# Optimization experiments

Hardware: AMD Instinct MI355X
Metric: run time of the kernel (lower is better)

## Reference

```python
import jax, jax.numpy as jnp
import numpy as np

N, IN_F, OUT_F = 65536, 512, 512


def setup_inputs() -> dict:
    key = jax.random.key(0)
    k1, k2, k3 = jax.random.split(key, 3)
    # Activations arrive as dequant-pending uint8-valued floats in [0, 256).
    x = jax.random.randint(k1, (N, IN_F), 0, 256).astype(jnp.float32)
    weight = jax.random.randint(k2, (OUT_F, IN_F), 0, 256).astype(jnp.int32)
    bias = jax.random.randint(k3, (OUT_F,), -512, 512).astype(jnp.int32)
    return {
        "x": x,
        "weight": weight,
        "bias": bias,
        "M": jnp.asarray(0.0123, dtype=jnp.float32),
        "x_zero": jnp.asarray(128.0, dtype=jnp.float32),
        "w_zero": jnp.asarray(128.0, dtype=jnp.float32),
        "y_zero": jnp.asarray(128.0, dtype=jnp.float32),
    }


def reference(x, weight, bias, M, x_zero, w_zero, y_zero):
    # y = round(linear(x - x_zero, w - w_zero, b) * M + y_zero)
    xs = x - x_zero                                   # [N, IN_F]
    w = weight.astype(jnp.float32) - w_zero           # [OUT_F, IN_F]
    y = jnp.einsum("ni,oi->no", xs, w) + bias.astype(jnp.float32)
    return jnp.round(y * M + y_zero)
```

## Files before the change

kernel.cpp:

```cpp
#include <hip/hip_runtime.h>


#define K_DIM 512
#define OUTF  512
#define NT    8
#define LDAB  80
#define TILE_B (128 * LDAB)
#define BUF_B  (2 * TILE_B)

typedef __attribute__((ext_vector_type(4))) int   i32x4;
typedef __attribute__((ext_vector_type(4))) float f32x4;

__global__ void wprep(const int* __restrict__ W, unsigned int* __restrict__ Wb,
                      const float* __restrict__ wzp) {
    const int wz = __float2int_rn(wzp[0]);
    int idx = (blockIdx.x * blockDim.x + threadIdx.x) * 4;
    i32x4 w = *reinterpret_cast<const i32x4*>(W + idx);
    unsigned int p = ((unsigned int)(w[0] - wz) & 0xffu)
                   | (((unsigned int)(w[1] - wz) & 0xffu) << 8)
                   | (((unsigned int)(w[2] - wz) & 0xffu) << 16)
                   | (((unsigned int)(w[3] - wz) & 0xffu) << 24);
    Wb[idx >> 2] = p;
}

__global__ __launch_bounds__(512, 4)
void qgemm(const float* __restrict__ X,
           const unsigned char* __restrict__ Wb,
           const int* __restrict__ bias,
           const float* __restrict__ Mp,
           const float* __restrict__ xzp,
           const float* __restrict__ yzp,
           float* __restrict__ Y) {
    __shared__ unsigned char lds[2 * BUF_B];

    const int tid  = threadIdx.x;
    const int lane = tid & 63;
    const int wid  = tid >> 6;
    const int wr   = wid >> 2;
    const int wc   = wid & 3;
    const int fr   = lane & 15;
    const int fq   = lane >> 4;

    const int b = blockIdx.x;
    const int lid = (b & 7) * 256 + (b >> 3);
    const int row0 = (lid >> 2) * 128;
    const int n0   = (lid & 3) * 128;

    const int xz = __float2int_rn(xzp[0]);

    const int srow = tid >> 2;
    const int scol = (tid & 3) * 16;
    const float* xbase = X + (size_t)(row0 + srow) * K_DIM + scol;
    const unsigned char* wbase = Wb + (size_t)(n0 + srow) * K_DIM + scol;
    const int aoff = srow * LDAB + scol;
    const int boff = TILE_B + srow * LDAB + scol;

    f32x4 ra[2][4];
    i32x4 rb[2];

    auto stage = [&](int t, int s) {
        const float* xp = xbase + t * 64;
        #pragma unroll
        for (int q = 0; q < 4; ++q)
            ra[s][q] = *reinterpret_cast<const f32x4*>(xp + q * 4);
        rb[s] = *reinterpret_cast<const i32x4*>(wbase + t * 64);
    };
    auto convwrite = [&](int buf, int s) {
        const int ab = buf * BUF_B;
        i32x4 pa;
        #pragma unroll
        for (int q = 0; q < 4; ++q) {
            unsigned int u0 = (unsigned int)((int)ra[s][q][0] - xz) & 0xffu;
            unsigned int u1 = (unsigned int)((int)ra[s][q][1] - xz) & 0xffu;
            unsigned int u2 = (unsigned int)((int)ra[s][q][2] - xz) & 0xffu;
            unsigned int u3 = (unsigned int)((int)ra[s][q][3] - xz) & 0xffu;
            pa[q] = (int)(u0 | (u1 << 8) | (u2 << 16) | (u3 << 24));
        }
        *reinterpret_cast<i32x4*>(&lds[ab + aoff]) = pa;
        *reinterpret_cast<i32x4*>(&lds[ab + boff]) = rb[s];
    };

    const int c0 = n0 + wc * 32;
    const int bv0 = bias[c0 + fr];
    const int bv1 = bias[c0 + 16 + fr];
    i32x4 acc[4][2];
    #pragma unroll
    for (int m = 0; m < 4; ++m) {
        acc[m][0] = i32x4{bv0, bv0, bv0, bv0};
        acc[m][1] = i32x4{bv1, bv1, bv1, bv1};
    }

    const int aro = (wr * 64 + fr) * LDAB + fq * 16;
    const int bro = TILE_B + (wc * 32 + fr) * LDAB + fq * 16;

    auto compute = [&](int buf) {
        const int ab = buf * BUF_B;
        i32x4 af[4], bf[2];
        #pragma unroll
        for (int m = 0; m < 4; ++m)
            af[m] = *reinterpret_cast<const i32x4*>(&lds[ab + aro + m * 16 * LDAB]);
        #pragma unroll
        for (int n = 0; n < 2; ++n)
            bf[n] = *reinterpret_cast<const i32x4*>(&lds[ab + bro + n * 16 * LDAB]);
        #pragma unroll
        for (int m = 0; m < 4; ++m)
            #pragma unroll
            for (int n = 0; n < 2; ++n)
                acc[m][n] = __builtin_amdgcn_mfma_i32_16x16x64_i8(
                    af[m], bf[n], acc[m][n], 0, 0, 0);
    };

    stage(0, 0);
    stage(1, 1);
    convwrite(0, 0);
    __syncthreads();

    #pragma unroll
    for (int t = 0; t < NT; ++t) {
        if (t + 2 < NT) stage(t + 2, t & 1);
        compute(t & 1);
        if (t + 1 < NT) convwrite((t + 1) & 1, (t + 1) & 1);
        __syncthreads();
    }

    const float Mv = Mp[0], yz = yzp[0];
    #pragma unroll
    for (int n = 0; n < 2; ++n) {
        const int col = c0 + n * 16 + fr;
        #pragma unroll
        for (int m = 0; m < 4; ++m) {
            const int row = row0 + wr * 64 + m * 16 + fq * 4;
            float* yp = Y + (size_t)row * OUTF + col;
            #pragma unroll
            for (int j = 0; j < 4; ++j)
                __builtin_nontemporal_store(
                    rintf((float)acc[m][n][j] * Mv + yz), yp + (size_t)j * OUTF);
        }
    }
}

extern "C" void kernel_launch(void* const* d_in, const int* in_sizes, int n_in,
                              void* d_out, int out_size, void* d_ws, size_t ws_size,
                              hipStream_t stream) {
    const float* x    = (const float*)d_in[0];
    const int*   w    = (const int*)d_in[1];
    const int*   bias = (const int*)d_in[2];
    const float* M    = (const float*)d_in[3];
    const float* xz   = (const float*)d_in[4];
    const float* wz   = (const float*)d_in[5];
    const float* yz   = (const float*)d_in[6];
    float* y = (float*)d_out;

    unsigned int* Wb = (unsigned int*)d_ws;

    wprep<<<256, 256, 0, stream>>>(w, Wb, wz);
    qgemm<<<2048, 512, 0, stream>>>(x, (const unsigned char*)Wb, bias, M, xz, yz, y);
}
```

Before: 68.67 us.

## Retile GEMM to 64-row blocks with full-width N and weights read from global

Each block now handles 64 rows across all 512 output columns, with each wave owning 64 columns. The weight fragments are loaded straight from global/L2 instead of being staged through LDS. The A tile is written to LDS in an MFMA-fragment-ordered layout so every lane reads a contiguous 16 bytes, and the barrier is replaced with an explicit lgkmcnt wait plus s_barrier. The aim is to read X exactly once, shrink LDS traffic and remove padding, but each wave now fetches weights from cache on every k-step and register pressure rises with 16 accumulators. Nontemporal stores are also dropped in favour of plain stores.

```diff
diff --git a/kernel.cpp b/kernel.cpp
--- a/kernel.cpp
+++ b/kernel.cpp
@@ -4,12 +4,10 @@
 #define K_DIM 512
 #define OUTF  512
 #define NT    8
-#define LDAB  80
-#define TILE_B (128 * LDAB)
-#define BUF_B  (2 * TILE_B)
 
 typedef __attribute__((ext_vector_type(4))) int   i32x4;
 typedef __attribute__((ext_vector_type(4))) float f32x4;
+typedef __attribute__((ext_vector_type(2))) unsigned int u32x2;
 
 __global__ void wprep(const int* __restrict__ W, unsigned int* __restrict__ Wb,
                       const float* __restrict__ wzp) {
@@ -31,110 +29,100 @@
            const float* __restrict__ xzp,
            const float* __restrict__ yzp,
            float* __restrict__ Y) {
-    __shared__ unsigned char lds[2 * BUF_B];
+    __shared__ unsigned char lds[2][4096];
 
     const int tid  = threadIdx.x;
     const int lane = tid & 63;
     const int wid  = tid >> 6;
-    const int wr   = wid >> 2;
-    const int wc   = wid & 3;
     const int fr   = lane & 15;
     const int fq   = lane >> 4;
 
-    const int b = blockIdx.x;
-    const int lid = (b & 7) * 256 + (b >> 3);
-    const int row0 = (lid >> 2) * 128;
-    const int n0   = (lid & 3) * 128;
+    const int row0 = blockIdx.x * 64;
+    const int c0   = wid * 64;
 
-    const int xz = __float2int_rn(xzp[0]);
+    const float xzf = xzp[0];
 
-    const int srow = tid >> 2;
-    const int scol = (tid & 3) * 16;
-    const float* xbase = X + (size_t)(row0 + srow) * K_DIM + scol;
-    const unsigned char* wbase = Wb + (size_t)(n0 + srow) * K_DIM + scol;
-    const int aoff = srow * LDAB + scol;
-    const int boff = TILE_B + srow * LDAB + scol;
+    const int srow = tid >> 3;
+    const int sk   = (tid & 7) * 8;
+    const float* xbase = X + (size_t)(row0 + srow) * K_DIM + sk;
+    const int ldst = (srow >> 4) * 1024 + ((srow & 15) + ((sk >> 4) << 4)) * 16 + (sk & 8);
 
-    f32x4 ra[2][4];
-    i32x4 rb[2];
+    f32x4 ra[2][2];
 
-    auto stage = [&](int t, int s) {
-        const float* xp = xbase + t * 64;
-        #pragma unroll
-        for (int q = 0; q < 4; ++q)
-            ra[s][q] = *reinterpret_cast<const f32x4*>(xp + q * 4);
-        rb[s] = *reinterpret_cast<const i32x4*>(wbase + t * 64);
+    auto stageA = [&](int t, int s) {
+        const float* p = xbase + t * 64;
+        ra[s][0] = *reinterpret_cast<const f32x4*>(p);
+        ra[s][1] = *reinterpret_cast<const f32x4*>(p + 4);
     };
     auto convwrite = [&](int buf, int s) {
-        const int ab = buf * BUF_B;
-        i32x4 pa;
+        u32x2 v;
         #pragma unroll
-        for (int q = 0; q < 4; ++q) {
-            unsigned int u0 = (unsigned int)((int)ra[s][q][0] - xz) & 0xffu;
-            unsigned int u1 = (unsigned int)((int)ra[s][q][1] - xz) & 0xffu;
-            unsigned int u2 = (unsigned int)((int)ra[s][q][2] - xz) & 0xffu;
-            unsigned int u3 = (unsigned int)((int)ra[s][q][3] - xz) & 0xffu;
-            pa[q] = (int)(u0 | (u1 << 8) | (u2 << 16) | (u3 << 24));
+        for (int h = 0; h < 2; ++h) {
+            unsigned int u0 = (unsigned int)((int)(ra[s][h][0] - xzf)) & 0xffu;
+            unsigned int u1 = (unsigned int)((int)(ra[s][h][1] - xzf)) & 0xffu;
+            unsigned int u2 = (unsigned int)((int)(ra[s][h][2] - xzf)) & 0xffu;
+            unsigned int u3 = (unsigned int)((int)(ra[s][h][3] - xzf)) & 0xffu;
+            v[h] = u0 | (u1 << 8) | (u2 << 16) | (u3 << 24);
         }
-        *reinterpret_cast<i32x4*>(&lds[ab + aoff]) = pa;
-        *reinterpret_cast<i32x4*>(&lds[ab + boff]) = rb[s];
+        *reinterpret_cast<u32x2*>(&lds[buf][ldst]) = v;
     };
 
-    const int c0 = n0 + wc * 32;
-    const int bv0 = bias[c0 + fr];
-    const int bv1 = bias[c0 + 16 + fr];
-    i32x4 acc[4][2];
+    i32x4 acc[4][4];
     #pragma unroll
-    for (int m = 0; m < 4; ++m) {
-        acc[m][0] = i32x4{bv0, bv0, bv0, bv0};
-        acc[m][1] = i32x4{bv1, bv1, bv1, bv1};
+    for (int n = 0; n < 4; ++n) {
+        const int bv = bias[c0 + n * 16 + fr];
+        #pragma unroll
+        for (int m = 0; m < 4; ++m)
+            acc[m][n] = i32x4{bv, bv, bv, bv};
     }
 
-    const int aro = (wr * 64 + fr) * LDAB + fq * 16;
-    const int bro = TILE_B + (wc * 32 + fr) * LDAB + fq * 16;
+    const unsigned char* wbb = Wb + (size_t)(c0 + fr) * K_DIM + fq * 16;
 
-    auto compute = [&](int buf) {
-        const int ab = buf * BUF_B;
-        i32x4 af[4], bf[2];
+    auto compute = [&](int buf, int ks) {
+        i32x4 af[4], bf[4];
         #pragma unroll
         for (int m = 0; m < 4; ++m)
-            af[m] = *reinterpret_cast<const i32x4*>(&lds[ab + aro + m * 16 * LDAB]);
+            af[m] = *reinterpret_cast<const i32x4*>(&lds[buf][m * 1024 + lane * 16]);
         #pragma unroll
-        for (int n = 0; n < 2; ++n)
-            bf[n] = *reinterpret_cast<const i32x4*>(&lds[ab + bro + n * 16 * LDAB]);
+        for (int n = 0; n < 4; ++n)
+            bf[n] = *reinterpret_cast<const i32x4*>(wbb + (size_t)n * 16 * K_DIM + ks * 64);
         #pragma unroll
         for (int m = 0; m < 4; ++m)
             #pragma unroll
-            for (int n = 0; n < 2; ++n)
+            for (int n = 0; n < 4; ++n)
                 acc[m][n] = __builtin_amdgcn_mfma_i32_16x16x64_i8(
                     af[m], bf[n], acc[m][n], 0, 0, 0);
     };
 
-    stage(0, 0);
-    stage(1, 1);
+    auto barrier = [&]() {
+        asm volatile("s_waitcnt lgkmcnt(0)" ::: "memory");
+        __builtin_amdgcn_s_barrier();
+    };
+
+    stageA(0, 0);
+    stageA(1, 1);
     convwrite(0, 0);
-    __syncthreads();
+    barrier();
 
     #pragma unroll
     for (int t = 0; t < NT; ++t) {
-        if (t + 2 < NT) stage(t + 2, t & 1);
-        compute(t & 1);
+        if (t + 2 < NT) stageA(t + 2, t & 1);
+        compute(t & 1, t);
         if (t + 1 < NT) convwrite((t + 1) & 1, (t + 1) & 1);
-        __syncthreads();
+        barrier();
     }
 
     const float Mv = Mp[0], yz = yzp[0];
     #pragma unroll
-    for (int n = 0; n < 2; ++n) {
+    for (int n = 0; n < 4; ++n) {
         const int col = c0 + n * 16 + fr;
         #pragma unroll
         for (int m = 0; m < 4; ++m) {
-            const int row = row0 + wr * 64 + m * 16 + fq * 4;
+            const int row = row0 + m * 16 + fq * 4;
             float* yp = Y + (size_t)row * OUTF + col;
             #pragma unroll
             for (int j = 0; j < 4; ++j)
-                __builtin_nontemporal_store(
-                    rintf((float)acc[m][n][j] * Mv + yz), yp + (size_t)j * OUTF);
+                yp[(size_t)j * OUTF] = rintf((float)acc[m][n][j] * Mv + yz);
         }
     }
 }
@@ -154,5 +142,5 @@
     unsigned int* Wb = (unsigned int*)d_ws;
 
     wprep<<<256, 256, 0, stream>>>(w, Wb, wz);
-    qgemm<<<2048, 512, 0, stream>>>(x, (const unsigned char*)Wb, bias, M, xz, yz, y);
+    qgemm<<<1024, 512, 0, stream>>>(x, (const unsigned char*)Wb, bias, M, xz, yz, y);
 }
```

Result: slower. 78.66 us (+14.5%).

## Store LDS tiles in MFMA fragment order and use a lighter barrier

Applied to the files above, without the earlier changes.

Each thread now loads a global chunk whose row and k position match an MFMA fragment slot, and writes it contiguously at tid*16 in LDS. Compute then reads each fragment as lane*16 from a 1 KB block, replacing the padded LDAB=80 layout. This is meant to make LDS reads and writes conflict-free with simple addressing. Three smaller changes ride along: __syncthreads is replaced by an lgkmcnt wait plus s_barrier, which skips the vmcnt wait so global prefetches can stay in flight. The zero-point subtraction moves to float, and the output stores are no longer nontemporal, which may change cache behaviour.

```diff
diff --git a/kernel.cpp b/kernel.cpp
--- a/kernel.cpp
+++ b/kernel.cpp
@@ -4,9 +4,6 @@
 #define K_DIM 512
 #define OUTF  512
 #define NT    8
-#define LDAB  80
-#define TILE_B (128 * LDAB)
-#define BUF_B  (2 * TILE_B)
 
 typedef __attribute__((ext_vector_type(4))) int   i32x4;
 typedef __attribute__((ext_vector_type(4))) float f32x4;
@@ -31,7 +28,7 @@
            const float* __restrict__ xzp,
            const float* __restrict__ yzp,
            float* __restrict__ Y) {
-    __shared__ unsigned char lds[2 * BUF_B];
+    __shared__ unsigned char lds[2][16384];
 
     const int tid  = threadIdx.x;
     const int lane = tid & 63;
@@ -46,38 +43,39 @@
     const int row0 = (lid >> 2) * 128;
     const int n0   = (lid & 3) * 128;
 
-    const int xz = __float2int_rn(xzp[0]);
+    const float xzf = xzp[0];
 
-    const int srow = tid >> 2;
-    const int scol = (tid & 3) * 16;
-    const float* xbase = X + (size_t)(row0 + srow) * K_DIM + scol;
-    const unsigned char* wbase = Wb + (size_t)(n0 + srow) * K_DIM + scol;
-    const int aoff = srow * LDAB + scol;
-    const int boff = TILE_B + srow * LDAB + scol;
+    const int trow = ((tid >> 6) << 4) + (tid & 15);
+    const int tk   = ((tid >> 4) & 3) * 16;
+    const float* xbase = X + (size_t)(row0 + trow) * K_DIM + tk;
+    const unsigned char* wbase = Wb + (size_t)(n0 + trow) * K_DIM + tk;
+    const int dA = tid * 16;
+    const int dB = 8192 + tid * 16;
 
     f32x4 ra[2][4];
     i32x4 rb[2];
 
-    auto stage = [&](int t, int s) {
+    auto stage = [&](int t) {
+        const int s = t & 1;
         const float* xp = xbase + t * 64;
         #pragma unroll
         for (int q = 0; q < 4; ++q)
             ra[s][q] = *reinterpret_cast<const f32x4*>(xp + q * 4);
         rb[s] = *reinterpret_cast<const i32x4*>(wbase + t * 64);
     };
-    auto convwrite = [&](int buf, int s) {
-        const int ab = buf * BUF_B;
+    auto convwrite = [&](int t) {
+        const int s = t & 1;
         i32x4 pa;
         #pragma unroll
         for (int q = 0; q < 4; ++q) {
-            unsigned int u0 = (unsigned int)((int)ra[s][q][0] - xz) & 0xffu;
-            unsigned int u1 = (unsigned int)((int)ra[s][q][1] - xz) & 0xffu;
-            unsigned int u2 = (unsigned int)((int)ra[s][q][2] - xz) & 0xffu;
-            unsigned int u3 = (unsigned int)((int)ra[s][q][3] - xz) & 0xffu;
+            unsigned int u0 = (unsigned int)((int)(ra[s][q][0] - xzf)) & 0xffu;
+            unsigned int u1 = (unsigned int)((int)(ra[s][q][1] - xzf)) & 0xffu;
+            unsigned int u2 = (unsigned int)((int)(ra[s][q][2] - xzf)) & 0xffu;
+            unsigned int u3 = (unsigned int)((int)(ra[s][q][3] - xzf)) & 0xffu;
             pa[q] = (int)(u0 | (u1 << 8) | (u2 << 16) | (u3 << 24));
         }
-        *reinterpret_cast<i32x4*>(&lds[ab + aoff]) = pa;
-        *reinterpret_cast<i32x4*>(&lds[ab + boff]) = rb[s];
+        *reinterpret_cast<i32x4*>(&lds[s][dA]) = pa;
+        *reinterpret_cast<i32x4*>(&lds[s][dB]) = rb[s];
     };
 
     const int c0 = n0 + wc * 32;
@@ -90,18 +88,15 @@
         acc[m][1] = i32x4{bv1, bv1, bv1, bv1};
     }
 
-    const int aro = (wr * 64 + fr) * LDAB + fq * 16;
-    const int bro = TILE_B + (wc * 32 + fr) * LDAB + fq * 16;
-
-    auto compute = [&](int buf) {
-        const int ab = buf * BUF_B;
+    auto compute = [&](int t) {
+        const int s = t & 1;
         i32x4 af[4], bf[2];
         #pragma unroll
         for (int m = 0; m < 4; ++m)
-            af[m] = *reinterpret_cast<const i32x4*>(&lds[ab + aro + m * 16 * LDAB]);
+            af[m] = *reinterpret_cast<const i32x4*>(&lds[s][(wr * 4 + m) * 1024 + lane * 16]);
         #pragma unroll
         for (int n = 0; n < 2; ++n)
-            bf[n] = *reinterpret_cast<const i32x4*>(&lds[ab + bro + n * 16 * LDAB]);
+            bf[n] = *reinterpret_cast<const i32x4*>(&lds[s][8192 + (wc * 2 + n) * 1024 + lane * 16]);
         #pragma unroll
         for (int m = 0; m < 4; ++m)
             #pragma unroll
@@ -110,17 +105,22 @@
                     af[m], bf[n], acc[m][n], 0, 0, 0);
     };
 
-    stage(0, 0);
-    stage(1, 1);
-    convwrite(0, 0);
-    __syncthreads();
+    auto barrier = [&]() {
+        asm volatile("s_waitcnt lgkmcnt(0)" ::: "memory");
+        __builtin_amdgcn_s_barrier();
+    };
+
+    stage(0);
+    stage(1);
+    convwrite(0);
+    barrier();
 
     #pragma unroll
     for (int t = 0; t < NT; ++t) {
-        if (t + 2 < NT) stage(t + 2, t & 1);
-        compute(t & 1);
-        if (t + 1 < NT) convwrite((t + 1) & 1, (t + 1) & 1);
-        __syncthreads();
+        if (t + 2 < NT) stage(t + 2);
+        compute(t);
+        if (t + 1 < NT) convwrite(t + 1);
+        barrier();
     }
 
     const float Mv = Mp[0], yz = yzp[0];
@@ -133,8 +133,7 @@
             float* yp = Y + (size_t)row * OUTF + col;
             #pragma unroll
             for (int j = 0; j < 4; ++j)
-                __builtin_nontemporal_store(
-                    rintf((float)acc[m][n][j] * Mv + yz), yp + (size_t)j * OUTF);
+                yp[(size_t)j * OUTF] = rintf((float)acc[m][n][j] * Mv + yz);
         }
     }
 }
```

Result: slower. 97.65 us (+42.2%).

## Pre-quantize X to int8 in a separate pass and load tiles directly into LDS

Applied to the files above, without the earlier changes.

Adds an xprep kernel that converts the float activations to zero-point-shifted int8 in workspace. A new qgemm then uses 64x64 output tiles, pulling the full K extent of X and W straight into LDS with global_load_lds, followed by a single sync and the MFMA loop. The old pipelined kernel is kept as a fallback when the workspace is too small, and the nontemporal output stores become plain stores. The cost is an extra full pass over X (read 128MB, write 32MB) plus smaller tiles with less data reuse, in exchange for removing the in-loop conversion and the register-to-LDS staging.

```diff
diff --git a/kernel.cpp b/kernel.cpp
--- a/kernel.cpp
+++ b/kernel.cpp
@@ -3,13 +3,16 @@
 
 #define K_DIM 512
 #define OUTF  512
-#define NT    8
-#define LDAB  80
-#define TILE_B (128 * LDAB)
-#define BUF_B  (2 * TILE_B)
 
 typedef __attribute__((ext_vector_type(4))) int   i32x4;
 typedef __attribute__((ext_vector_type(4))) float f32x4;
+typedef __attribute__((ext_vector_type(4))) unsigned int u32x4;
+
+__device__ __forceinline__ void gload16(const void* g, void* l) {
+    __builtin_amdgcn_global_load_lds(
+        (const __attribute__((address_space(1))) void*)g,
+        (__attribute__((address_space(3))) void*)l, 16, 0, 0);
+}
 
 __global__ void wprep(const int* __restrict__ W, unsigned int* __restrict__ Wb,
                       const float* __restrict__ wzp) {
@@ -23,14 +26,101 @@
     Wb[idx >> 2] = p;
 }
 
+__global__ __launch_bounds__(256)
+void xprep(const float* __restrict__ X, u32x4* __restrict__ Xb,
+           const float* __restrict__ xzp) {
+    const float xzf = xzp[0];
+    size_t i = (size_t)blockIdx.x * blockDim.x + threadIdx.x;
+    const f32x4* xp = reinterpret_cast<const f32x4*>(X) + i * 4;
+    u32x4 o;
+    #pragma unroll
+    for (int q = 0; q < 4; ++q) {
+        f32x4 v = xp[q];
+        unsigned int b0 = (unsigned int)((int)(v[0] - xzf)) & 0xffu;
+        unsigned int b1 = (unsigned int)((int)(v[1] - xzf)) & 0xffu;
+        unsigned int b2 = (unsigned int)((int)(v[2] - xzf)) & 0xffu;
+        unsigned int b3 = (unsigned int)((int)(v[3] - xzf)) & 0xffu;
+        o[q] = b0 | (b1 << 8) | (b2 << 16) | (b3 << 24);
+    }
+    Xb[i] = o;
+}
+
 __global__ __launch_bounds__(512, 4)
-void qgemm(const float* __restrict__ X,
+void qgemm(const unsigned char* __restrict__ Xb,
            const unsigned char* __restrict__ Wb,
            const int* __restrict__ bias,
            const float* __restrict__ Mp,
-           const float* __restrict__ xzp,
            const float* __restrict__ yzp,
            float* __restrict__ Y) {
+    __shared__ unsigned char lds[65536];
+
+    const int tid  = threadIdx.x;
+    const int lane = tid & 63;
+    const int wid  = tid >> 6;
+    const int fr   = lane & 15;
+    const int fq   = lane >> 4;
+
+    const int b   = blockIdx.x;
+    const int q   = b >> 3;
+    const int rp  = (b & 7) * 128 + (q >> 3);
+    const int row0 = rp * 64;
+    const int c0t  = (q & 7) * 64;
+
+    if (wid < 4) {
+        const unsigned char* g = Xb + (size_t)(row0 + wid * 16 + fr) * K_DIM + fq * 16;
+        #pragma unroll
+        for (int ks = 0; ks < 8; ++ks)
+            gload16(g + ks * 64, &lds[(wid * 8 + ks) * 1024]);
+    } else {
+        const int n = wid - 4;
+        const unsigned char* g = Wb + (size_t)(c0t + n * 16 + fr) * K_DIM + fq * 16;
+        #pragma unroll
+        for (int ks = 0; ks < 8; ++ks)
+            gload16(g + ks * 64, &lds[32768 + (n * 8 + ks) * 1024]);
+    }
+
+    const int wrow = wid >> 1;
+    const int wcn  = (wid & 1) * 2;
+    const int col0 = c0t + wcn * 16 + fr;
+    const int bv0 = bias[col0];
+    const int bv1 = bias[col0 + 16];
+    i32x4 acc0 = {bv0, bv0, bv0, bv0};
+    i32x4 acc1 = {bv1, bv1, bv1, bv1};
+
+    __syncthreads();
+
+    #pragma unroll
+    for (int ks = 0; ks < 8; ++ks) {
+        i32x4 af = *reinterpret_cast<const i32x4*>(&lds[(wrow * 8 + ks) * 1024 + lane * 16]);
+        i32x4 b0 = *reinterpret_cast<const i32x4*>(&lds[32768 + (wcn * 8 + ks) * 1024 + lane * 16]);
+        i32x4 b1 = *reinterpret_cast<const i32x4*>(&lds[32768 + ((wcn + 1) * 8 + ks) * 1024 + lane * 16]);
+        acc0 = __builtin_amdgcn_mfma_i32_16x16x64_i8(af, b0, acc0, 0, 0, 0);
+        acc1 = __builtin_amdgcn_mfma_i32_16x16x64_i8(af, b1, acc1, 0, 0, 0);
+    }
+
+    const float Mv = Mp[0], yz = yzp[0];
+    const int row = row0 + wrow * 16 + fq * 4;
+    float* yp = Y + (size_t)row * OUTF + col0;
+    #pragma unroll
+    for (int j = 0; j < 4; ++j) {
+        yp[(size_t)j * OUTF]      = rintf((float)acc0[j] * Mv + yz);
+        yp[(size_t)j * OUTF + 16] = rintf((float)acc1[j] * Mv + yz);
+    }
+}
+
+#define NT    8
+#define LDAB  80
+#define TILE_B (128 * LDAB)
+#define BUF_B  (2 * TILE_B)
+
+__global__ __launch_bounds__(512, 4)
+void qgemm_fb(const float* __restrict__ X,
+              const unsigned char* __restrict__ Wb,
+              const int* __restrict__ bias,
+              const float* __restrict__ Mp,
+              const float* __restrict__ xzp,
+              const float* __restrict__ yzp,
+              float* __restrict__ Y) {
     __shared__ unsigned char lds[2 * BUF_B];
 
     const int tid  = threadIdx.x;
@@ -46,7 +136,7 @@
     const int row0 = (lid >> 2) * 128;
     const int n0   = (lid & 3) * 128;
 
-    const int xz = __float2int_rn(xzp[0]);
+    const float xzf = xzp[0];
 
     const int srow = tid >> 2;
     const int scol = (tid & 3) * 16;
@@ -58,23 +148,25 @@
     f32x4 ra[2][4];
     i32x4 rb[2];
 
-    auto stage = [&](int t, int s) {
+    auto stage = [&](int t) {
+        const int s = t & 1;
         const float* xp = xbase + t * 64;
         #pragma unroll
-        for (int q = 0; q < 4; ++q)
-            ra[s][q] = *reinterpret_cast<const f32x4*>(xp + q * 4);
+        for (int qq = 0; qq < 4; ++qq)
+            ra[s][qq] = *reinterpret_cast<const f32x4*>(xp + qq * 4);
         rb[s] = *reinterpret_cast<const i32x4*>(wbase + t * 64);
     };
-    auto convwrite = [&](int buf, int s) {
+    auto convwrite = [&](int t, int buf) {
+        const int s = t & 1;
         const int ab = buf * BUF_B;
         i32x4 pa;
         #pragma unroll
-        for (int q = 0; q < 4; ++q) {
-            unsigned int u0 = (unsigned int)((int)ra[s][q][0] - xz) & 0xffu;
-            unsigned int u1 = (unsigned int)((int)ra[s][q][1] - xz) & 0xffu;
-            unsigned int u2 = (unsigned int)((int)ra[s][q][2] - xz) & 0xffu;
-            unsigned int u3 = (unsigned int)((int)ra[s][q][3] - xz) & 0xffu;
-            pa[q] = (int)(u0 | (u1 << 8) | (u2 << 16) | (u3 << 24));
+        for (int qq = 0; qq < 4; ++qq) {
+            unsigned int u0 = (unsigned int)((int)(ra[s][qq][0] - xzf)) & 0xffu;
+            unsigned int u1 = (unsigned int)((int)(ra[s][qq][1] - xzf)) & 0xffu;
+            unsigned int u2 = (unsigned int)((int)(ra[s][qq][2] - xzf)) & 0xffu;
+            unsigned int u3 = (unsigned int)((int)(ra[s][qq][3] - xzf)) & 0xffu;
+            pa[qq] = (int)(u0 | (u1 << 8) | (u2 << 16) | (u3 << 24));
         }
         *reinterpret_cast<i32x4*>(&lds[ab + aoff]) = pa;
         *reinterpret_cast<i32x4*>(&lds[ab + boff]) = rb[s];
@@ -110,16 +202,16 @@
                     af[m], bf[n], acc[m][n], 0, 0, 0);
     };
 
-    stage(0, 0);
-    stage(1, 1);
+    stage(0);
+    stage(1);
     convwrite(0, 0);
     __syncthreads();
 
     #pragma unroll
     for (int t = 0; t < NT; ++t) {
-        if (t + 2 < NT) stage(t + 2, t & 1);
+        if (t + 2 < NT) stage(t + 2);
         compute(t & 1);
-        if (t + 1 < NT) convwrite((t + 1) & 1, (t + 1) & 1);
+        if (t + 1 < NT) convwrite(t + 1, (t + 1) & 1);
         __syncthreads();
     }
 
@@ -133,8 +225,7 @@
             float* yp = Y + (size_t)row * OUTF + col;
             #pragma unroll
             for (int j = 0; j < 4; ++j)
-                __builtin_nontemporal_store(
-                    rintf((float)acc[m][n][j] * Mv + yz), yp + (size_t)j * OUTF);
+                yp[(size_t)j * OUTF] = rintf((float)acc[m][n][j] * Mv + yz);
         }
     }
 }
@@ -151,8 +242,16 @@
     const float* yz   = (const float*)d_in[6];
     float* y = (float*)d_out;
 
-    unsigned int* Wb = (unsigned int*)d_ws;
-
-    wprep<<<256, 256, 0, stream>>>(w, Wb, wz);
-    qgemm<<<2048, 512, 0, stream>>>(x, (const unsigned char*)Wb, bias, M, xz, yz, y);
-}
+    unsigned char* Wb  = (unsigned char*)d_ws;
+    unsigned char* Xbp = Wb + 256 * 1024;
+    const size_t need = 256 * 1024 + (size_t)65536 * 512;
+
+    wprep<<<256, 256, 0, stream>>>(w, (unsigned int*)Wb, wz);
+
+    if (ws_size >= need) {
+        xprep<<<8192, 256, 0, stream>>>(x, (u32x4*)Xbp, xz);
+        qgemm<<<8192, 512, 0, stream>>>(Xbp, Wb, bias, M, yz, y);
+    } else {
+        qgemm_fb<<<2048, 512, 0, stream>>>(x, Wb, bias, M, xz, yz, y);
+    }
+}
```

After: 108.1 us. 57.4% more time.
